# Performance work log

Measured on AMD Instinct MI355X. Metric: run time of the kernel, lower is better.

## Reference

```python
import jax, jax.numpy as jnp
import numpy as np
from jax import lax

MAX_DEPTH = 8
NLEAVES = 2 ** MAX_DEPTH      # 256
NNODES = 2 ** MAX_DEPTH - 1   # 255 (preorder-numbered inner nodes)
NCLASS = 10
EPS = 1e-5
BATCH = 8192


def _build_paths():
    # Reproduce the torch preorder node numbering and DFS leaf numbering.
    node_ctr = [0]
    leaf_paths = []
    def rec(depth, path):
        idx = node_ctr[0]; node_ctr[0] += 1
        if depth < MAX_DEPTH:
            rec(depth + 1, path + [(idx, 0)])   # left child: prob (1 - p)
            rec(depth + 1, path + [(idx, 1)])   # right child: prob p
        else:
            leaf_paths.append(path + [(idx, 0)])
            leaf_paths.append(path + [(idx, 1)])
    rec(1, [])
    nidx = np.array([[n for n, _ in p] for p in leaf_paths], dtype=np.int32)  # [L, D]
    dirs = np.array([[d for _, d in p] for p in leaf_paths], dtype=bool)      # [L, D]
    return nidx, dirs

NODE_IDX, DIRS = _build_paths()


def _bn(x, g, b):
    # training-mode batchnorm over all dims except channel axis 1 (biased var)
    axes = tuple(i for i in range(x.ndim) if i != 1)
    m = x.mean(axes, keepdims=True)
    v = x.var(axes, keepdims=True)
    shape = [1] * x.ndim; shape[1] = -1
    return (x - m) * lax.rsqrt(v + EPS) * g.reshape(shape) + b.reshape(shape)


def _conv(x, w, b):
    y = lax.conv_general_dilated(x, w, (1, 1), 'VALID',
                                 dimension_numbers=('NCHW', 'OIHW', 'NCHW'))
    return y + b[None, :, None, None]


def _pool2(x):
    return lax.reduce_window(x, -jnp.inf, lax.max, (1, 1, 2, 2), (1, 1, 2, 2), 'VALID')


def setup_inputs() -> dict:
    ks = jax.random.split(jax.random.key(0), 12)
    f32 = jnp.float32
    return {
        'x': jax.random.normal(ks[0], (BATCH, 1, 28, 28), f32),
        'y': jax.random.randint(ks[1], (BATCH,), 0, NCLASS),
        'conv1_w': 0.1 * jax.random.normal(ks[2], (20, 1, 5, 5), f32),
        'conv1_b': jnp.zeros((20,), f32),
        'conv2_w': 0.05 * jax.random.normal(ks[3], (50, 20, 5, 5), f32),
        'conv2_b': jnp.zeros((50,), f32),
        'g1': jnp.ones((20,), f32), 'be1': jnp.zeros((20,), f32),
        'g2': jnp.ones((50,), f32), 'be2': jnp.zeros((50,), f32),
        'fc1_w': 0.05 * jax.random.normal(ks[4], (10, 800), f32),
        'fc1_b': jnp.zeros((10,), f32),
        'g3': jnp.ones((10,), f32), 'be3': jnp.zeros((10,), f32),
        'theta_w': 0.3 * jax.random.normal(ks[5], (NNODES, 10), f32),
        'theta_b': jnp.zeros((NNODES,), f32),
        'pi': jax.random.uniform(ks[6], (NLEAVES, NCLASS), f32, 0.1, 1.0),
    }


def reference(x, y, conv1_w, conv1_b, conv2_w, conv2_b, g1, be1, g2, be2,
              fc1_w, fc1_b, g3, be3, theta_w, theta_b, pi):
    B = x.shape[0]
    # CNN backbone
    h = _pool2(jax.nn.relu(_bn(_conv(x, conv1_w, conv1_b), g1, be1)))
    h = _pool2(jax.nn.relu(_bn(_conv(h, conv2_w, conv2_b), g2, be2)))
    h = h.reshape(B, 4 * 4 * 50)
    h = jax.nn.relu(_bn(h @ fc1_w.T + fc1_b, g3, be3))        # [B, 10]
    # batched soft-tree gating: one fused GEMM for all 255 tiny Linear(10,1)
    p = jax.nn.sigmoid(h @ theta_w.T + theta_b)                # [B, NNODES]
    g = p[:, NODE_IDX]                                         # [B, L, D]
    mu = jnp.prod(jnp.where(DIRS[None], g, 1.0 - g), axis=2)   # [B, L]
    # pi is a row-stochastic distribution (uniform at torch init)
    pi_n = pi / pi.sum(1, keepdims=True)
    # stale P from __init__: uniform mu (1/L) @ pi  ->  column means of pi
    P_prev = jnp.broadcast_to(pi_n.mean(0), (B, NCLASS))       # [B, C]
    # vectorized cal_pi (soft-EM update of leaf distributions)
    Y = jax.nn.one_hot(y, NCLASS, dtype=mu.dtype)              # [B, C]
    S = mu.T @ (Y / P_prev)                                    # [L, C]
    pi_h = pi_n * S
    pi_new = pi_h / pi_h.sum(1, keepdims=True)
    # cal_P and log
    P = mu @ pi_new                                            # [B, C]
    return jnp.log(P)
```

## Files before the change

### kernel.cpp

```cpp
#include <hip/hip_runtime.h>
#include <hip/hip_bf16.h>
#include <math.h>

typedef __attribute__((ext_vector_type(8))) short short8v;
typedef __attribute__((ext_vector_type(4))) float float4v;

static const size_t F_RAWP1B = 0;
static const size_t F_C2P    = 14155776;
static const size_t F_PART1  = 20709376;
static const size_t F_PART2  = 21037056;
static const size_t F_PART3  = 21241856;
static const size_t F_BN1    = 21246976;
static const size_t F_BN2    = 21247016;
static const size_t F_BN3    = 21247116;
static const size_t F_SRAW   = 21247136;
static const size_t F_PINEW  = 21249696;
static const size_t F_WB2    = 21252256;
static const size_t F_WB1    = 21271712;
static const size_t F_SPART  = 21272224;
static const size_t F_HRAW   = 0;
static const size_t F_MU     = 81920;

__device__ __forceinline__ float relu_(float v) { return v > 0.f ? v : 0.f; }

__device__ __forceinline__ unsigned int pack_bf16x2(float a, float b) {
  __hip_bfloat16 ha = __float2bfloat16(a), hb = __float2bfloat16(b);
  unsigned short ua, ub;
  __builtin_memcpy(&ua, &ha, 2); __builtin_memcpy(&ub, &hb, 2);
  return ((unsigned int)ub << 16) | ua;
}

__device__ __forceinline__ unsigned short cvt_bf16(float a) {
  __hip_bfloat16 h = __float2bfloat16(a);
  unsigned short u; __builtin_memcpy(&u, &h, 2);
  return u;
}

__device__ __forceinline__ float pick_(float a, float b, bool mx) {
  return mx ? fmaxf(a, b) : fminf(a, b);
}

__global__ __launch_bounds__(256) void k_wprep1(
    const float* __restrict__ w, unsigned short* __restrict__ wb1)
{
  const int i = blockIdx.x * 256 + threadIdx.x;
  const int n = i >> 5, k = i & 31;
  const int kh = k / 6, kw = k - kh*6;
  float v = (n < 20 && kh < 5 && kw < 5) ? w[n*25 + kh*5 + kw] : 0.f;
  wb1[i] = cvt_bf16(v);
}

__global__ __launch_bounds__(256) void k_wprep2(
    const float* __restrict__ w, unsigned short* __restrict__ wb)
{
  const int idx = blockIdx.x * 256 + threadIdx.x;
  const int cc = idx >> 9;
  const int rem = idx & 511;
  const int n = rem >> 3, j = rem & 7;
  float v = 0.f;
  if (cc < 75 && n < 50) {
    const int khw = cc / 3, icg = cc - khw*3;
    const int ic = icg*8 + j;
    if (ic < 20) {
      const int kh = khw / 5, kw = khw - kh*5;
      v = w[((n*20 + ic)*5 + kh)*5 + kw];
    }
  }
  wb[idx] = cvt_bf16(v);
}

__global__ __launch_bounds__(256) void k_conv1_mfma(
    const float* __restrict__ x, const unsigned short* __restrict__ wb1,
    const float* __restrict__ g1, unsigned int* __restrict__ rawp1b,
    float* __restrict__ part)
{
  __shared__ alignas(16) unsigned short xpk[2][1568];
  __shared__ float sred[4][32], qred[4][32];
  const int tid = threadIdx.x, blk = blockIdx.x;
  const int img0 = blk * 4;
  const int wave = tid >> 6, lane = tid & 63, lo = lane & 15, hi = lane >> 4;

  const short8v bfr0 = *(const short8v*)(wb1 + (lo*32 + hi*8));
  const short8v bfr1 = *(const short8v*)(wb1 + ((16+lo)*32 + hi*8));
  const unsigned enc = (hi==0) ? 0x0E020100u
                     : (hi==1) ? 0x1D1C100Fu
                     : (hi==2) ? 0x2C2B2A1Eu
                     :           0x003A3938u;
  const int off0 = enc & 255, off1 = (enc>>8)&255, off2 = (enc>>16)&255, off3 = enc>>24;
  const int pb   = (lo & 1) * 392;
  const int oyp  = (lo >> 1) & 1, qoff = lo >> 2;
  const int inv  = pb + (6*wave + oyp)*14;
  const bool gp0 = (g1[lo] >= 0.f);
  const bool gp1 = (lo < 4) ? (g1[16+lo] >= 0.f) : true;
  const int r0 = tid / 28,        c0 = tid - r0*28;
  const int r1 = (tid+256) / 28,  c1 = (tid+256) - r1*28;
  const int r2 = (tid+512) / 28,  c2 = (tid+512) - r2*28;
  const int r3 = (tid+768) / 28,  c3 = (tid+768) - r3*28;

  float st0, st1, st2, st3;
  {
    const float* xp = x + (size_t)img0 * 784;
    st0 = xp[tid]; st1 = xp[tid+256]; st2 = xp[tid+512];
    st3 = (tid < 16) ? xp[tid+768] : 0.f;
  }
  {
    unsigned short* b0 = &xpk[0][0];
    const unsigned short u0 = cvt_bf16(st0), u1 = cvt_bf16(st1), u2 = cvt_bf16(st2);
    b0[r0*28 + c0] = u0;
    if (c0 >= 1) b0[784 + r0*28 + c0 - 1] = u0; else b0[784 + r0*28 + 27] = 0;
    b0[r1*28 + c1] = u1;
    if (c1 >= 1) b0[784 + r1*28 + c1 - 1] = u1; else b0[784 + r1*28 + 27] = 0;
    b0[r2*28 + c2] = u2;
    if (c2 >= 1) b0[784 + r2*28 + c2 - 1] = u2; else b0[784 + r2*28 + 27] = 0;
    if (tid < 16) {
      const unsigned short u3 = cvt_bf16(st3);
      b0[r3*28 + c3] = u3;
      if (c3 >= 1) b0[784 + r3*28 + c3 - 1] = u3;
    }
  }
  __syncthreads();

  float bsv0 = 0.f, bqv0 = 0.f, bsv1 = 0.f, bqv1 = 0.f;
  int cur = 0;
  for (int ii = 0; ii < 4; ++ii) {
    if (ii < 3) {
      const float* xp = x + (size_t)(img0 + ii + 1) * 784;
      st0 = xp[tid]; st1 = xp[tid+256]; st2 = xp[tid+512];
      st3 = (tid < 16) ? xp[tid+768] : 0.f;
    }
    const unsigned int* xpd = (const unsigned int*)&xpk[cur][0];
    float4v acc[9][2];
    #pragma unroll
    for (int t = 0; t < 9; ++t) {
      acc[t][0] = (float4v){0.f,0.f,0.f,0.f};
      acc[t][1] = (float4v){0.f,0.f,0.f,0.f};
    }
    #pragma unroll
    for (int tt = 0; tt < 9; ++tt) {
      const int pylc = (tt*4) / 12;
      const int pxlc = (tt*4) - pylc*12;
      const int base = inv + pylc*28 + pxlc + qoff;
      union { unsigned int u[4]; short8v v; } cu;
      cu.u[0] = xpd[base + off0];
      cu.u[1] = xpd[base + off1];
      cu.u[2] = xpd[base + off2];
      cu.u[3] = xpd[base + off3];
      acc[tt][0] = __builtin_amdgcn_mfma_f32_16x16x32_bf16(cu.v, bfr0, acc[tt][0], 0, 0, 0);
      acc[tt][1] = __builtin_amdgcn_mfma_f32_16x16x32_bf16(cu.v, bfr1, acc[tt][1], 0, 0, 0);
    }
    unsigned int* dst = rawp1b + (size_t)(img0 + ii) * 1728;
    #pragma unroll
    for (int tt = 0; tt < 9; ++tt) {
      const int T = wave*9 + tt;
      const int q = T*4 + hi;
      const float4v v0 = acc[tt][0];
      const float4v v1 = acc[tt][1];
      #pragma unroll
      for (int r = 0; r < 4; ++r) { bsv0 += v0[r]; bqv0 += v0[r]*v0[r]; }
      #pragma unroll
      for (int r = 0; r < 4; ++r) { bsv1 += v1[r]; bqv1 += v1[r]*v1[r]; }
      const float p0 = pick_(pick_(v0[0], v0[1], gp0), pick_(v0[2], v0[3], gp0), gp0);
      const float p1 = pick_(pick_(v1[0], v1[1], gp1), pick_(v1[2], v1[3], gp1), gp1);
      const float o0 = __shfl_down(p0, 1);
      const float o1 = __shfl_down(p1, 1);
      if ((lo & 1) == 0) {
        dst[q*12 + (lo >> 1)] = pack_bf16x2(p0, o0);
        if (lo < 8)
          dst[q*12 + 8 + (lo >> 1)] = pack_bf16x2(p1, o1);
      }
    }
    if (ii < 3) {
      unsigned short* bn = &xpk[cur ^ 1][0];
      const unsigned short u0 = cvt_bf16(st0), u1 = cvt_bf16(st1), u2 = cvt_bf16(st2);
      bn[r0*28 + c0] = u0;
      if (c0 >= 1) bn[784 + r0*28 + c0 - 1] = u0; else bn[784 + r0*28 + 27] = 0;
      bn[r1*28 + c1] = u1;
      if (c1 >= 1) bn[784 + r1*28 + c1 - 1] = u1; else bn[784 + r1*28 + 27] = 0;
      bn[r2*28 + c2] = u2;
      if (c2 >= 1) bn[784 + r2*28 + c2 - 1] = u2; else bn[784 + r2*28 + 27] = 0;
      if (tid < 16) {
        const unsigned short u3 = cvt_bf16(st3);
        bn[r3*28 + c3] = u3;
        if (c3 >= 1) bn[784 + r3*28 + c3 - 1] = u3;
      }
    }
    __syncthreads();
    cur ^= 1;
  }

  bsv0 += __shfl_down(bsv0, 32); bqv0 += __shfl_down(bqv0, 32);
  bsv0 += __shfl_down(bsv0, 16); bqv0 += __shfl_down(bqv0, 16);
  bsv1 += __shfl_down(bsv1, 32); bqv1 += __shfl_down(bqv1, 32);
  bsv1 += __shfl_down(bsv1, 16); bqv1 += __shfl_down(bqv1, 16);
  if (hi == 0) {
    sred[wave][lo] = bsv0; sred[wave][16+lo] = bsv1;
    qred[wave][lo] = bqv0; qred[wave][16+lo] = bqv1;
  }
  __syncthreads();
  if (tid < 20) {
    float s = 0.f, q = 0.f;
    #pragma unroll
    for (int w2 = 0; w2 < 4; ++w2) { s += sred[w2][tid]; q += qred[w2][tid]; }
    part[(size_t)blk*40 + tid]      = s;
    part[(size_t)blk*40 + 20 + tid] = q;
  }
}

__global__ __launch_bounds__(256) void k_conv2_mfma(
    const unsigned int* __restrict__ rawp1b, const unsigned short* __restrict__ wb,
    const float* __restrict__ bn1, const float* __restrict__ g2,
    float* __restrict__ c2p, float* __restrict__ part)
{
  __shared__ alignas(16) unsigned int in4[6912];
  __shared__ float sred[4][64], qred[4][64];
  __shared__ alignas(16) float bn1i[48];
  __shared__ unsigned short aofft[76];
  const int tid = threadIdx.x, blk = blockIdx.x;
  if (tid < 24) {
    const float sc = (tid < 20) ? bn1[tid]      : 0.f;
    const float sh = (tid < 20) ? bn1[20 + tid] : 0.f;
    bn1i[2*tid] = sc; bn1i[2*tid + 1] = sh;
  }
  if (tid < 76) {
    const int cc2 = tid > 74 ? 74 : tid;
    const int khw = cc2 / 3, icg = cc2 - khw*3;
    const int kh = khw / 5, kw = khw - kh*5;
    aofft[tid] = (unsigned short)((kh*12 + kw)*48 + icg*16);
  }
  __syncthreads();

  const uint4* src4 = (const uint4*)(rawp1b + (size_t)blk * 6912);
  uint4* dst4 = (uint4*)in4;
  int jj = tid % 3;
  for (int k = 0; k < 7; ++k) {
    const int i = k*256 + tid;
    if (i < 1728) {
      const uint4 v = src4[i];
      unsigned int o[4];
      #pragma unroll
      for (int m = 0; m < 4; ++m) {
        const float4 ss = *(const float4*)(bn1i + jj*16 + m*4);
        const unsigned int u = (m==0) ? v.x : (m==1) ? v.y : (m==2) ? v.z : v.w;
        const float a = __uint_as_float(u << 16);
        const float b = __uint_as_float(u & 0xffff0000u);
        const float ra = relu_(fmaf(a, ss.x, ss.y));
        const float rb = relu_(fmaf(b, ss.z, ss.w));
        o[m] = pack_bf16x2(ra, rb);
      }
      uint4 ov; ov.x = o[0]; ov.y = o[1]; ov.z = o[2]; ov.w = o[3];
      dst4[i] = ov;
    }
    jj = (jj == 2) ? 0 : jj + 1;
  }
  __syncthreads();

  const int wave = tid >> 6, lane = tid & 63;
  const int lo = lane & 15, hi = lane >> 4;
  const char* ibase = (const char*)in4 + wave * 6912;

  const char* bA[4];
  #pragma unroll
  for (int a = 0; a < 4; ++a) {
    const int m = a*16 + lo;
    bA[a] = ibase + ((m >> 3) * 12 + (m & 7)) * 48;
  }
  unsigned short aoffs[19];
  #pragma unroll
  for (int s = 0; s < 19; ++s) aoffs[s] = aofft[s*4 + hi];
  const unsigned short* wbase = wb + hi*512 + lo*8;

  bool gpos[4];
  #pragma unroll
  for (int nf = 0; nf < 4; ++nf) {
    const int n = nf*16 + lo;
    gpos[nf] = (n < 50) ? (g2[n] >= 0.f) : true;
  }

  float4v acc[4][4];
  #pragma unroll
  for (int a = 0; a < 4; ++a)
    #pragma unroll
    for (int nf = 0; nf < 4; ++nf) acc[a][nf] = (float4v){0.f, 0.f, 0.f, 0.f};

  #pragma unroll
  for (int s = 0; s < 19; ++s) {
    short8v av[4], bv[4];
    #pragma unroll
    for (int am = 0; am < 4; ++am)
      av[am] = *(const short8v*)(bA[am] + aoffs[s]);
    const unsigned short* wrow = wbase + s*2048;
    #pragma unroll
    for (int nf = 0; nf < 4; ++nf)
      bv[nf] = *(const short8v*)(wrow + nf*128);
    #pragma unroll
    for (int am = 0; am < 4; ++am)
      #pragma unroll
      for (int nf = 0; nf < 4; ++nf)
        acc[am][nf] = __builtin_amdgcn_mfma_f32_16x16x32_bf16(av[am], bv[nf], acc[am][nf], 0, 0, 0);
  }

  const int img = blk*4 + wave;
  #pragma unroll
  for (int nf = 0; nf < 4; ++nf) {
    const int n = nf*16 + lo;
    float sv = 0.f, qv = 0.f;
    #pragma unroll
    for (int am = 0; am < 4; ++am) {
      float4v v = acc[am][nf];
      #pragma unroll
      for (int r = 0; r < 4; ++r) { sv += v[r]; qv += v[r]*v[r]; }
      float h0 = gpos[nf] ? fmaxf(v[0], v[1]) : fminf(v[0], v[1]);
      float h1 = gpos[nf] ? fmaxf(v[2], v[3]) : fminf(v[2], v[3]);
      const float o0 = __shfl_xor(h0, 32);
      const float o1 = __shfl_xor(h1, 32);
      h0 = gpos[nf] ? fmaxf(h0, o0) : fminf(h0, o0);
      h1 = gpos[nf] ? fmaxf(h1, o1) : fminf(h1, o1);
      if (hi < 2 && n < 50) {
        float2 o; o.x = h0; o.y = h1;
        *(float2*)(c2p + (size_t)img*800 + n*16 + am*4 + hi*2) = o;
      }
    }
    sv += __shfl_down(sv, 32); qv += __shfl_down(qv, 32);
    sv += __shfl_down(sv, 16); qv += __shfl_down(qv, 16);
    if (hi == 0) { sred[wave][nf*16 + lo] = sv; qred[wave][nf*16 + lo] = qv; }
  }
  __syncthreads();
  if (tid < 100) {
    const int ch = tid < 50 ? tid : tid - 50;
    float t = 0.f;
    if (tid < 50) {
      #pragma unroll
      for (int w2 = 0; w2 < 4; ++w2) t += sred[w2][ch];
      part[(size_t)blk*100 + ch] = t;
    } else {
      #pragma unroll
      for (int w2 = 0; w2 < 4; ++w2) t += qred[w2][ch];
      part[(size_t)blk*100 + 50 + ch] = t;
    }
  }
}

__global__ __launch_bounds__(256) void k_bn_fin(
    const float* __restrict__ part, int nblk, int nch, float N,
    const float* __restrict__ g, const float* __restrict__ b,
    float* __restrict__ out)
{
  __shared__ double rd[4][2];
  const int tid = threadIdx.x, ch = blockIdx.x;
  const int lane = tid & 63, wid = tid >> 6;
  double s = 0.0, q = 0.0;
  for (int i = tid; i < nblk; i += 256) {
    s += (double)part[(size_t)i*2*nch + ch];
    q += (double)part[(size_t)i*2*nch + nch + ch];
  }
  #pragma unroll
  for (int off = 32; off > 0; off >>= 1) { s += __shfl_down(s, off); q += __shfl_down(q, off); }
  if (lane == 0) { rd[wid][0] = s; rd[wid][1] = q; }
  __syncthreads();
  if (tid == 0) {
    double S = rd[0][0] + rd[1][0] + rd[2][0] + rd[3][0];
    double Q = rd[0][1] + rd[1][1] + rd[2][1] + rd[3][1];
    double mean = S / (double)N;
    double var  = Q / (double)N - mean * mean;
    if (var < 0.0) var = 0.0;
    float scv = (float)((double)g[ch] / sqrt(var + 1e-5));
    out[ch]       = scv;
    out[nch + ch] = b[ch] - (float)mean * scv;
  }
}

__global__ __launch_bounds__(256) void k_fc1(
    const float* __restrict__ c2p, const float* __restrict__ bn2,
    const float* __restrict__ fw, float* __restrict__ h_raw,
    float* __restrict__ part)
{
  __shared__ alignas(16) float wl[8000];
  __shared__ float s2[50], h2[50];
  __shared__ float red[4][20];
  const int tid = threadIdx.x;
  for (int i = tid; i < 2000; i += 256)
    ((float4*)wl)[i] = ((const float4*)fw)[i];
  if (tid < 50) { s2[tid] = bn2[tid]; h2[tid] = bn2[50 + tid]; }
  __syncthreads();
  const int s = tid >> 3, kc = tid & 7;
  const int sample = blockIdx.x * 32 + s;
  const float* xr = c2p + (size_t)sample * 800 + kc * 100;
  float acc[10];
  #pragma unroll
  for (int f = 0; f < 10; ++f) acc[f] = 0.f;
  #pragma unroll 5
  for (int c = 0; c < 25; ++c) {
    const int k = kc*100 + c*4;
    float4 v = *(const float4*)(xr + c*4);
    const int oc = k >> 4;
    const float sc = s2[oc], sh = h2[oc];
    v.x = relu_(v.x*sc + sh); v.y = relu_(v.y*sc + sh);
    v.z = relu_(v.z*sc + sh); v.w = relu_(v.w*sc + sh);
    #pragma unroll
    for (int f = 0; f < 10; ++f) {
      const float4 wv = *(const float4*)(wl + f*800 + k);
      acc[f] += v.x*wv.x + v.y*wv.y + v.z*wv.z + v.w*wv.w;
    }
  }
  const int lane = tid & 63, wid = tid >> 6;
  #pragma unroll
  for (int f = 0; f < 10; ++f) {
    acc[f] += __shfl_down(acc[f], 4);
    acc[f] += __shfl_down(acc[f], 2);
    acc[f] += __shfl_down(acc[f], 1);
    float a2 = (kc == 0) ? acc[f] : 0.f;
    float q2 = (kc == 0) ? acc[f]*acc[f] : 0.f;
    if (kc == 0) h_raw[(size_t)sample*10 + f] = acc[f];
    a2 += __shfl_down(a2, 32); q2 += __shfl_down(q2, 32);
    a2 += __shfl_down(a2, 16); q2 += __shfl_down(q2, 16);
    a2 += __shfl_down(a2, 8);  q2 += __shfl_down(q2, 8);
    if (lane == 0) { red[wid][f] = a2; red[wid][10+f] = q2; }
  }
  __syncthreads();
  if (tid < 20) {
    float t = 0.f;
    #pragma unroll
    for (int w2 = 0; w2 < 4; ++w2) t += red[w2][tid];
    part[(size_t)blockIdx.x*20 + tid] = t;
  }
}

__global__ __launch_bounds__(256) void k_theta_mu(
    const float* __restrict__ h_raw, const float* __restrict__ bn3,
    const float* __restrict__ tw, const float* __restrict__ tb,
    float* __restrict__ mu)
{
  __shared__ float twt[10][256];
  __shared__ float tbl[256];
  __shared__ float hl[32][10];
  __shared__ float pl[32][256];
  const int tid = threadIdx.x, blk = blockIdx.x;
  for (int i = tid; i < 2550; i += 256) {
    const int node = i / 10, f = i - node*10;
    twt[f][node] = tw[i];
  }
  if (tid < 10) twt[tid][255] = 0.f;
  tbl[tid] = (tid < 255) ? tb[tid] : 0.f;
  for (int i = tid; i < 320; i += 256) {
    const int ss = i / 10, f = i - ss*10;
    hl[ss][f] = relu_(h_raw[(size_t)blk*320 + i] * bn3[f] + bn3[10 + f]);
  }
  __syncthreads();
  const int node = tid;
  for (int i2 = 0; i2 < 32; ++i2) {
    float h[10];
    #pragma unroll
    for (int f = 0; f < 10; ++f) h[f] = hl[i2][f];
    float d = tbl[node];
    #pragma unroll
    for (int f = 0; f < 10; ++f) d += h[f] * twt[f][node];
    pl[i2][node] = (node < 255) ? 1.f / (1.f + __expf(-d)) : 0.f;
  }
  __syncthreads();
  for (int i2 = 0; i2 < 32; ++i2) {
    float m = 1.f; int idx = 0;
    #pragma unroll
    for (int k = 0; k < 8; ++k) {
      const int dir = (tid >> (7 - k)) & 1;
      const float pv = pl[i2][idx];
      m *= dir ? pv : (1.f - pv);
      idx += dir ? (1 << (7 - k)) : 1;
    }
    mu[(size_t)(blk*32 + i2)*256 + tid] = m;
  }
}

__global__ __launch_bounds__(256) void k_S_part(
    const float* __restrict__ mu, const int* __restrict__ y,
    float* __restrict__ spart)
{
  const int tid = threadIdx.x;
  const int b0 = blockIdx.x * 32;
  float acc[10];
  #pragma unroll
  for (int c = 0; c < 10; ++c) acc[c] = 0.f;
  for (int s = 0; s < 32; ++s) {
    const int b = b0 + s;
    const float m = mu[(size_t)b*256 + tid];
    const int c = y[b];
    #pragma unroll
    for (int cc = 0; cc < 10; ++cc) acc[cc] += (c == cc) ? m : 0.f;
  }
  float* dst = spart + (size_t)blockIdx.x*2560 + tid*10;
  #pragma unroll
  for (int cc = 0; cc < 10; ++cc) dst[cc] = acc[cc];
}

__global__ __launch_bounds__(256) void k_S_red(
    const float* __restrict__ spart, float* __restrict__ S)
{
  const int e = blockIdx.x * 256 + threadIdx.x;
  float s = 0.f;
  for (int k = 0; k < 256; ++k) s += spart[(size_t)k*2560 + e];
  S[e] = s;
}

__global__ __launch_bounds__(256) void k_pi(
    const float* __restrict__ pi, const float* __restrict__ S,
    float* __restrict__ pi_new)
{
  __shared__ float pin[2560];
  __shared__ float Pp[10];
  const int t = threadIdx.x;
  float row[10]; float rs = 0.f;
  #pragma unroll
  for (int c = 0; c < 10; ++c) { row[c] = pi[t*10 + c]; rs += row[c]; }
  #pragma unroll
  for (int c = 0; c < 10; ++c) { row[c] /= rs; pin[t*10 + c] = row[c]; }
  __syncthreads();
  if (t < 10) {
    float s = 0.f;
    for (int l = 0; l < 256; ++l) s += pin[l*10 + t];
    Pp[t] = s / 256.f;
  }
  __syncthreads();
  float hs = 0.f; float ph[10];
  #pragma unroll
  for (int c = 0; c < 10; ++c) {
    const float Sv = S[t*10 + c] / Pp[c];
    ph[c] = row[c] * Sv;
    hs += ph[c];
  }
  #pragma unroll
  for (int c = 0; c < 10; ++c) pi_new[t*10 + c] = ph[c] / hs;
}

__global__ __launch_bounds__(256) void k_out(
    const float* __restrict__ mu, const float* __restrict__ pn,
    float* __restrict__ out)
{
  __shared__ float plt[10][260];
  const int tid = threadIdx.x;
  if (tid < 256) {
    #pragma unroll
    for (int c = 0; c < 10; ++c) plt[c][tid] = pn[tid*10 + c];
  }
  __syncthreads();
  const int gid = blockIdx.x * 256 + tid;
  const int b = gid / 10, c = gid % 10;
  const float4* mr4 = (const float4*)(mu + (size_t)b * 256);
  const float*  pc  = &plt[c][0];
  float a0 = 0.f, a1 = 0.f;
  #pragma unroll 4
  for (int l4 = 0; l4 < 64; ++l4) {
    const float4 m = mr4[l4];
    const float4 p = *(const float4*)(pc + 4*l4);
    a0 += m.x*p.x + m.y*p.y;
    a1 += m.z*p.z + m.w*p.w;
  }
  out[gid] = logf(a0 + a1);
}

extern "C" void kernel_launch(void* const* d_in, const int* in_sizes, int n_in,
                              void* d_out, int out_size, void* d_ws, size_t ws_size,
                              hipStream_t stream)
{
  const float* x   = (const float*)d_in[0];
  const int*   y   = (const int*)  d_in[1];
  const float* c1w = (const float*)d_in[2];
  const float* c2w = (const float*)d_in[4];
  const float* g1  = (const float*)d_in[6];
  const float* be1 = (const float*)d_in[7];
  const float* g2  = (const float*)d_in[8];
  const float* be2 = (const float*)d_in[9];
  const float* fw  = (const float*)d_in[10];
  const float* g3  = (const float*)d_in[12];
  const float* be3 = (const float*)d_in[13];
  const float* thw = (const float*)d_in[14];
  const float* thb = (const float*)d_in[15];
  const float* pi  = (const float*)d_in[16];
  float* ws  = (float*)d_ws;
  float* out = (float*)d_out;

  unsigned int*   rawp1b = (unsigned int*)(ws + F_RAWP1B);
  float*          c2p    = ws + F_C2P;
  float*          part1  = ws + F_PART1;
  float*          part2  = ws + F_PART2;
  float*          part3  = ws + F_PART3;
  float*          bn1    = ws + F_BN1;
  float*          bn2    = ws + F_BN2;
  float*          bn3    = ws + F_BN3;
  float*          sraw   = ws + F_SRAW;
  float*          pinew  = ws + F_PINEW;
  unsigned short* wb2    = (unsigned short*)(ws + F_WB2);
  unsigned short* wb1    = (unsigned short*)(ws + F_WB1);
  float*          spart  = ws + F_SPART;
  float*          hraw   = ws + F_HRAW;
  float*          muB    = ws + F_MU;

  k_wprep1<<<4, 256, 0, stream>>>(c1w, wb1);
  k_wprep2<<<152, 256, 0, stream>>>(c2w, wb2);
  k_conv1_mfma<<<2048, 256, 0, stream>>>(x, wb1, g1, rawp1b, part1);
  k_bn_fin<<<20, 256, 0, stream>>>(part1, 2048, 20, 8192.f * 576.f, g1, be1, bn1);
  k_conv2_mfma<<<2048, 256, 0, stream>>>(rawp1b, wb2, bn1, g2, c2p, part2);
  k_bn_fin<<<50, 256, 0, stream>>>(part2, 2048, 50, 8192.f * 64.f, g2, be2, bn2);
  k_fc1<<<256, 256, 0, stream>>>(c2p, bn2, fw, hraw, part3);
  k_bn_fin<<<10, 256, 0, stream>>>(part3, 256, 10, 8192.f, g3, be3, bn3);
  k_theta_mu<<<256, 256, 0, stream>>>(hraw, bn3, thw, thb, muB);
  k_S_part<<<256, 256, 0, stream>>>(muB, y, spart);
  k_S_red<<<10, 256, 0, stream>>>(spart, sraw);
  k_pi<<<1, 256, 0, stream>>>(pi, sraw, pinew);
  k_out<<<320, 256, 0, stream>>>(muB, pinew, out);
}
```

Baseline: 175.0 us.

## Fuse small tail kernels: weight prep, BN3 finalize, S partials, pi update

Merges the two weight-prep kernels into one launch. The BN3 finalize now runs inside the theta/mu kernel, with each block redundantly reducing the 256 fc1 partials. The per-block S partial sums are accumulated in theta_mu, so mu is not re-read from global memory. The single-block pi update is folded into every k_out block, removing four launches in total. The cost is redundant per-block reductions of part3 and of pi in each block, plus extra register pressure in theta_mu.

```diff
diff --git a/kernel.cpp b/kernel.cpp
--- a/kernel.cpp
+++ b/kernel.cpp
@@ -12,9 +12,7 @@
 static const size_t F_PART3  = 21241856;
 static const size_t F_BN1    = 21246976;
 static const size_t F_BN2    = 21247016;
-static const size_t F_BN3    = 21247116;
 static const size_t F_SRAW   = 21247136;
-static const size_t F_PINEW  = 21249696;
 static const size_t F_WB2    = 21252256;
 static const size_t F_WB1    = 21271712;
 static const size_t F_SPART  = 21272224;
@@ -40,33 +38,32 @@
   return mx ? fmaxf(a, b) : fminf(a, b);
 }
 
-__global__ __launch_bounds__(256) void k_wprep1(
-    const float* __restrict__ w, unsigned short* __restrict__ wb1)
-{
-  const int i = blockIdx.x * 256 + threadIdx.x;
-  const int n = i >> 5, k = i & 31;
-  const int kh = k / 6, kw = k - kh*6;
-  float v = (n < 20 && kh < 5 && kw < 5) ? w[n*25 + kh*5 + kw] : 0.f;
-  wb1[i] = cvt_bf16(v);
-}
-
-__global__ __launch_bounds__(256) void k_wprep2(
-    const float* __restrict__ w, unsigned short* __restrict__ wb)
-{
-  const int idx = blockIdx.x * 256 + threadIdx.x;
-  const int cc = idx >> 9;
-  const int rem = idx & 511;
-  const int n = rem >> 3, j = rem & 7;
-  float v = 0.f;
-  if (cc < 75 && n < 50) {
-    const int khw = cc / 3, icg = cc - khw*3;
-    const int ic = icg*8 + j;
-    if (ic < 20) {
-      const int kh = khw / 5, kw = khw - kh*5;
-      v = w[((n*20 + ic)*5 + kh)*5 + kw];
-    }
-  }
-  wb[idx] = cvt_bf16(v);
+__global__ __launch_bounds__(256) void k_wprep(
+    const float* __restrict__ w1, const float* __restrict__ w2,
+    unsigned short* __restrict__ wb1, unsigned short* __restrict__ wb2)
+{
+  const int gi = blockIdx.x * 256 + threadIdx.x;
+  if (gi < 1024) {
+    const int n = gi >> 5, k = gi & 31;
+    const int kh = k / 6, kw = k - kh*6;
+    float v = (n < 20 && kh < 5 && kw < 5) ? w1[n*25 + kh*5 + kw] : 0.f;
+    wb1[gi] = cvt_bf16(v);
+  } else {
+    const int idx = gi - 1024;
+    const int cc = idx >> 9;
+    const int rem = idx & 511;
+    const int n = rem >> 3, j = rem & 7;
+    float v = 0.f;
+    if (cc < 75 && n < 50) {
+      const int khw = cc / 3, icg = cc - khw*3;
+      const int ic = icg*8 + j;
+      if (ic < 20) {
+        const int kh = khw / 5, kw = khw - kh*5;
+        v = w2[((n*20 + ic)*5 + kh)*5 + kw];
+      }
+    }
+    wb2[idx] = cvt_bf16(v);
+  }
 }
 
 __global__ __launch_bounds__(256) void k_conv1_mfma(
@@ -426,26 +423,65 @@
 }
 
 __global__ __launch_bounds__(256) void k_theta_mu(
-    const float* __restrict__ h_raw, const float* __restrict__ bn3,
+    const float* __restrict__ h_raw, const float* __restrict__ part3,
+    const float* __restrict__ g3, const float* __restrict__ be3,
     const float* __restrict__ tw, const float* __restrict__ tb,
-    float* __restrict__ mu)
+    const int* __restrict__ y, float* __restrict__ mu,
+    float* __restrict__ spart)
 {
   __shared__ float twt[10][256];
   __shared__ float tbl[256];
   __shared__ float hl[32][10];
   __shared__ float pl[32][256];
+  __shared__ float red3[4][20];
+  __shared__ float bn3s[20];
+  __shared__ int   ycls[32];
   const int tid = threadIdx.x, blk = blockIdx.x;
+  const int lane = tid & 63, wid = tid >> 6;
+
   for (int i = tid; i < 2550; i += 256) {
     const int node = i / 10, f = i - node*10;
     twt[f][node] = tw[i];
   }
   if (tid < 10) twt[tid][255] = 0.f;
   tbl[tid] = (tid < 255) ? tb[tid] : 0.f;
+  if (tid < 32) ycls[tid] = y[blk*32 + tid];
+
+  float p3[20];
+  {
+    const float* pr = part3 + (size_t)tid * 20;
+    #pragma unroll
+    for (int j = 0; j < 20; ++j) p3[j] = pr[j];
+    #pragma unroll
+    for (int off = 32; off > 0; off >>= 1) {
+      #pragma unroll
+      for (int j = 0; j < 20; ++j) p3[j] += __shfl_down(p3[j], off);
+    }
+    if (lane == 0) {
+      #pragma unroll
+      for (int j = 0; j < 20; ++j) red3[wid][j] = p3[j];
+    }
+  }
+  __syncthreads();
+  if (tid < 10) {
+    double S = 0.0, Q = 0.0;
+    #pragma unroll
+    for (int w2 = 0; w2 < 4; ++w2) { S += red3[w2][tid]; Q += red3[w2][10+tid]; }
+    double mean = S / 8192.0;
+    double var  = Q / 8192.0 - mean*mean;
+    if (var < 0.0) var = 0.0;
+    float scv = (float)((double)g3[tid] / sqrt(var + 1e-5));
+    bn3s[tid]      = scv;
+    bn3s[10 + tid] = be3[tid] - (float)mean * scv;
+  }
+  __syncthreads();
+
   for (int i = tid; i < 320; i += 256) {
     const int ss = i / 10, f = i - ss*10;
-    hl[ss][f] = relu_(h_raw[(size_t)blk*320 + i] * bn3[f] + bn3[10 + f]);
-  }
-  __syncthreads();
+    hl[ss][f] = relu_(h_raw[(size_t)blk*320 + i] * bn3s[f] + bn3s[10 + f]);
+  }
+  __syncthreads();
+
   const int node = tid;
   for (int i2 = 0; i2 < 32; ++i2) {
     float h[10];
@@ -457,6 +493,10 @@
     pl[i2][node] = (node < 255) ? 1.f / (1.f + __expf(-d)) : 0.f;
   }
   __syncthreads();
+
+  float sacc[10];
+  #pragma unroll
+  for (int c = 0; c < 10; ++c) sacc[c] = 0.f;
   for (int i2 = 0; i2 < 32; ++i2) {
     float m = 1.f; int idx = 0;
     #pragma unroll
@@ -467,28 +507,13 @@
       idx += dir ? (1 << (7 - k)) : 1;
     }
     mu[(size_t)(blk*32 + i2)*256 + tid] = m;
-  }
-}
-
-__global__ __launch_bounds__(256) void k_S_part(
-    const float* __restrict__ mu, const int* __restrict__ y,
-    float* __restrict__ spart)
-{
-  const int tid = threadIdx.x;
-  const int b0 = blockIdx.x * 32;
-  float acc[10];
-  #pragma unroll
-  for (int c = 0; c < 10; ++c) acc[c] = 0.f;
-  for (int s = 0; s < 32; ++s) {
-    const int b = b0 + s;
-    const float m = mu[(size_t)b*256 + tid];
-    const int c = y[b];
-    #pragma unroll
-    for (int cc = 0; cc < 10; ++cc) acc[cc] += (c == cc) ? m : 0.f;
-  }
-  float* dst = spart + (size_t)blockIdx.x*2560 + tid*10;
-  #pragma unroll
-  for (int cc = 0; cc < 10; ++cc) dst[cc] = acc[cc];
+    const int c = ycls[i2];
+    #pragma unroll
+    for (int cc = 0; cc < 10; ++cc) sacc[cc] += (c == cc) ? m : 0.f;
+  }
+  float* dst = spart + (size_t)blk*2560 + tid*10;
+  #pragma unroll
+  for (int cc = 0; cc < 10; ++cc) dst[cc] = sacc[cc];
 }
 
 __global__ __launch_bounds__(256) void k_S_red(
@@ -500,47 +525,46 @@
   S[e] = s;
 }
 
-__global__ __launch_bounds__(256) void k_pi(
-    const float* __restrict__ pi, const float* __restrict__ S,
-    float* __restrict__ pi_new)
-{
-  __shared__ float pin[2560];
-  __shared__ float Pp[10];
-  const int t = threadIdx.x;
+__global__ __launch_bounds__(256) void k_out(
+    const float* __restrict__ mu, const float* __restrict__ pi,
+    const float* __restrict__ S, float* __restrict__ out)
+{
+  __shared__ float plt[10][260];
+  __shared__ float wred[4][10];
+  const int tid = threadIdx.x;
+  const int lane = tid & 63, wid = tid >> 6;
+
   float row[10]; float rs = 0.f;
   #pragma unroll
-  for (int c = 0; c < 10; ++c) { row[c] = pi[t*10 + c]; rs += row[c]; }
-  #pragma unroll
-  for (int c = 0; c < 10; ++c) { row[c] /= rs; pin[t*10 + c] = row[c]; }
-  __syncthreads();
-  if (t < 10) {
-    float s = 0.f;
-    for (int l = 0; l < 256; ++l) s += pin[l*10 + t];
-    Pp[t] = s / 256.f;
+  for (int c = 0; c < 10; ++c) { row[c] = pi[tid*10 + c]; rs += row[c]; }
+  #pragma unroll
+  for (int c = 0; c < 10; ++c) row[c] /= rs;
+  float pp[10];
+  #pragma unroll
+  for (int c = 0; c < 10; ++c) pp[c] = row[c];
+  #pragma unroll
+  for (int off = 32; off > 0; off >>= 1) {
+    #pragma unroll
+    for (int c = 0; c < 10; ++c) pp[c] += __shfl_down(pp[c], off);
+  }
+  if (lane == 0) {
+    #pragma unroll
+    for (int c = 0; c < 10; ++c) wred[wid][c] = pp[c];
   }
   __syncthreads();
   float hs = 0.f; float ph[10];
   #pragma unroll
   for (int c = 0; c < 10; ++c) {
-    const float Sv = S[t*10 + c] / Pp[c];
+    const float Pp = (wred[0][c] + wred[1][c] + wred[2][c] + wred[3][c]) * (1.f/256.f);
+    const float Sv = S[tid*10 + c] / Pp;
     ph[c] = row[c] * Sv;
     hs += ph[c];
   }
-  #pragma unroll
-  for (int c = 0; c < 10; ++c) pi_new[t*10 + c] = ph[c] / hs;
-}
-
-__global__ __launch_bounds__(256) void k_out(
-    const float* __restrict__ mu, const float* __restrict__ pn,
-    float* __restrict__ out)
-{
-  __shared__ float plt[10][260];
-  const int tid = threadIdx.x;
-  if (tid < 256) {
-    #pragma unroll
-    for (int c = 0; c < 10; ++c) plt[c][tid] = pn[tid*10 + c];
-  }
-  __syncthreads();
+  const float ih = 1.f / hs;
+  #pragma unroll
+  for (int c = 0; c < 10; ++c) plt[c][tid] = ph[c] * ih;
+  __syncthreads();
+
   const int gid = blockIdx.x * 256 + tid;
   const int b = gid / 10, c = gid % 10;
   const float4* mr4 = (const float4*)(mu + (size_t)b * 256);
@@ -584,26 +608,20 @@
   float*          part3  = ws + F_PART3;
   float*          bn1    = ws + F_BN1;
   float*          bn2    = ws + F_BN2;
-  float*          bn3    = ws + F_BN3;
   float*          sraw   = ws + F_SRAW;
-  float*          pinew  = ws + F_PINEW;
   unsigned short* wb2    = (unsigned short*)(ws + F_WB2);
   unsigned short* wb1    = (unsigned short*)(ws + F_WB1);
   float*          spart  = ws + F_SPART;
   float*          hraw   = ws + F_HRAW;
   float*          muB    = ws + F_MU;
 
-  k_wprep1<<<4, 256, 0, stream>>>(c1w, wb1);
-  k_wprep2<<<152, 256, 0, stream>>>(c2w, wb2);
+  k_wprep<<<156, 256, 0, stream>>>(c1w, c2w, wb1, wb2);
   k_conv1_mfma<<<2048, 256, 0, stream>>>(x, wb1, g1, rawp1b, part1);
   k_bn_fin<<<20, 256, 0, stream>>>(part1, 2048, 20, 8192.f * 576.f, g1, be1, bn1);
   k_conv2_mfma<<<2048, 256, 0, stream>>>(rawp1b, wb2, bn1, g2, c2p, part2);
   k_bn_fin<<<50, 256, 0, stream>>>(part2, 2048, 50, 8192.f * 64.f, g2, be2, bn2);
   k_fc1<<<256, 256, 0, stream>>>(c2p, bn2, fw, hraw, part3);
-  k_bn_fin<<<10, 256, 0, stream>>>(part3, 256, 10, 8192.f, g3, be3, bn3);
-  k_theta_mu<<<256, 256, 0, stream>>>(hraw, bn3, thw, thb, muB);
-  k_S_part<<<256, 256, 0, stream>>>(muB, y, spart);
+  k_theta_mu<<<256, 256, 0, stream>>>(hraw, part3, g3, be3, thw, thb, y, muB, spart);
   k_S_red<<<10, 256, 0, stream>>>(spart, sraw);
-  k_pi<<<1, 256, 0, stream>>>(pi, sraw, pinew);
-  k_out<<<320, 256, 0, stream>>>(muB, pinew, out);
-}
+  k_out<<<320, 256, 0, stream>>>(muB, pi, sraw, out);
+}
```

New measurement: 171.2 us. 1.02x faster.
